# Performance work log

Measured on AMD Instinct MI355X. Metric: run time of the kernel, lower is better.

Reference implementation:

```python
import jax, jax.numpy as jnp
import numpy as np

N_NODES = 100000
N_EDGES = 3200000
NEG_SLOPE = 0.2  # PyG GATConv default


def setup_inputs() -> dict:
    key = jax.random.key(0)
    ks = jax.random.split(key, 10)
    g = 0.1
    return {
        "x": jax.random.normal(ks[0], (N_NODES, 3), jnp.float32),
        "edge_index": jax.random.randint(ks[1], (2, N_EDGES), 0, N_NODES),
        "w1": jax.random.normal(ks[2], (3, 32), jnp.float32) * g,
        "att_src1": jax.random.normal(ks[3], (2, 16), jnp.float32) * g,
        "att_dst1": jax.random.normal(ks[4], (2, 16), jnp.float32) * g,
        "b1": jnp.zeros((32,), jnp.float32),
        "w2": jax.random.normal(ks[5], (32, 14), jnp.float32) * g,
        "att_src2": jax.random.normal(ks[6], (2, 7), jnp.float32) * g,
        "att_dst2": jax.random.normal(ks[7], (2, 7), jnp.float32) * g,
        "b2": jnp.zeros((7,), jnp.float32),
    }


def _gat_conv(x, src, dst, W, att_src, att_dst, bias, heads, out_ch, concat, n):
    # x: [N, F_in]; src/dst: [E] (self-loops already appended)
    xl = (x @ W).reshape(n, heads, out_ch)          # [N, H, C]
    a_s = jnp.sum(xl * att_src[None], axis=-1)      # [N, H]
    a_d = jnp.sum(xl * att_dst[None], axis=-1)      # [N, H]
    alpha = jax.nn.leaky_relu(a_s[src] + a_d[dst], NEG_SLOPE)  # [E, H]
    # segment softmax over edges sharing a destination node
    mx = jax.ops.segment_max(alpha, dst, num_segments=n)        # [N, H]
    e = jnp.exp(alpha - mx[dst])
    denom = jax.ops.segment_sum(e, dst, num_segments=n)         # [N, H]
    alpha = e / (denom[dst] + 1e-16)
    msg = xl[src] * alpha[:, :, None]                            # [E, H, C]
    out = jax.ops.segment_sum(msg, dst, num_segments=n)         # [N, H, C]
    out = out.reshape(n, heads * out_ch) if concat else out.mean(axis=1)
    return out + bias


def reference(x, edge_index, w1, att_src1, att_dst1, b1, w2, att_src2, att_dst2, b2):
    n = x.shape[0]
    loop = jnp.arange(n)
    src = jnp.concatenate([edge_index[0], loop])  # add self-loops (PyG default)
    dst = jnp.concatenate([edge_index[1], loop])
    h = _gat_conv(x, src, dst, w1, att_src1, att_dst1, b1, 2, 16, True, n)
    h = jax.nn.relu(h)
    h = _gat_conv(h, src, dst, w2, att_src2, att_dst2, b2, 2, 7, False, n)
    return jax.nn.log_softmax(h, axis=1)
```

## Files before the change

kernel.cpp:

```cpp
#include <hip/hip_runtime.h>
#include <hip/hip_fp16.h>

static constexpr float NEG_SLOPE = 0.2f;
#define BUCKET_BITS 7
#define BNODES (1 << BUCKET_BITS)
#define MAXNB 1024
#define MAXSUP 32
#define SUPER_SHIFT 12
#define CHUNK1 2048
#define CHUNK 4096
#define PTHREADS 256
#define SORT_CAP 6144

__device__ __forceinline__ float2 h2f(float r) {
  return __half22float2(__builtin_bit_cast(__half2, r));
}

__global__ void k_node1(const float* __restrict__ x,
                        const float* __restrict__ w1,
                        const float* __restrict__ atts,
                        const float* __restrict__ attd,
                        float4* __restrict__ xp,
                        float* __restrict__ ad_,
                        unsigned* __restrict__ scur,
                        unsigned* __restrict__ bcur,
                        int n) {
  int i = blockIdx.x * blockDim.x + threadIdx.x;
  if (i < MAXSUP) scur[i] = 0u;
  if (i < MAXNB) bcur[i] = 0u;
  if (i >= n) return;
  float x0 = x[3*i], x1 = x[3*i+1], x2 = x[3*i+2];
  float v[32];
#pragma unroll
  for (int j = 0; j < 32; ++j)
    v[j] = fmaf(x0, w1[j], fmaf(x1, w1[32+j], x2 * w1[64+j]));
  float s0=0.f, s1=0.f, d0=0.f, d1=0.f;
#pragma unroll
  for (int k = 0; k < 16; ++k) {
    s0 = fmaf(v[k],    atts[k],    s0);
    d0 = fmaf(v[k],    attd[k],    d0);
    s1 = fmaf(v[16+k], atts[16+k], s1);
    d1 = fmaf(v[16+k], attd[16+k], d1);
  }
  float4 r;
  r.x = __builtin_bit_cast(float, __floats2half2_rn(x0, x1));
  r.y = __builtin_bit_cast(float, __floats2half2_rn(x2, s0));
  r.z = __builtin_bit_cast(float, __floats2half2_rn(s1, 0.f));
  r.w = 0.f;
  xp[i] = r;
  ad_[2*i] = d0; ad_[2*i+1] = d1;
}

__global__ void k_part1(const int* __restrict__ esrc, const int* __restrict__ edst,
                        unsigned* __restrict__ scur, unsigned* __restrict__ tmp1,
                        unsigned caps, int E) {
  __shared__ unsigned whist[4 * MAXSUP], wsub[4 * MAXSUP], woffs[4 * MAXSUP];
  int t = threadIdx.x;
  int w = t >> 6;
  for (int i = t; i < 4 * MAXSUP; i += PTHREADS) { whist[i] = 0u; woffs[i] = 0u; }
  __syncthreads();
  int e0 = blockIdx.x * CHUNK1;
  int e1 = min(E, e0 + CHUNK1);
  unsigned pkr[8], hir[8];
  int eb = e0 + t;
#pragma unroll
  for (int k = 0; k < 8; ++k) {
    int e = eb + k * PTHREADS;
    if (e < e1) {
      unsigned d = (unsigned)edst[e];
      unsigned s = (unsigned)esrc[e];
      unsigned hi = d >> SUPER_SHIFT;
      pkr[k] = (((d >> BUCKET_BITS) & 31u) << 24)
             | ((d & (BNODES - 1u)) << 17) | s;
      hir[k] = hi;
      atomicAdd(&whist[w * MAXSUP + hi], 1u);
    } else {
      hir[k] = 0xFFFFFFFFu;
    }
  }
  __syncthreads();
  if (t < MAXSUP) {
    unsigned h0 = whist[t],             h1 = whist[MAXSUP + t];
    unsigned h2 = whist[2*MAXSUP + t],  h3 = whist[3*MAXSUP + t];
    unsigned tot = h0 + h1 + h2 + h3;
    unsigned base = tot ? atomicAdd(&scur[t], tot) : 0u;
    wsub[t]            = base;
    wsub[MAXSUP + t]   = base + h0;
    wsub[2*MAXSUP + t] = base + h0 + h1;
    wsub[3*MAXSUP + t] = base + h0 + h1 + h2;
  }
  __syncthreads();
#pragma unroll
  for (int k = 0; k < 8; ++k) {
    unsigned hi = hir[k];
    if (hi != 0xFFFFFFFFu) {
      unsigned r = atomicAdd(&woffs[w * MAXSUP + hi], 1u);
      tmp1[(size_t)hi * caps + wsub[w * MAXSUP + hi] + r] = pkr[k];
    }
  }
}

__global__ void k_part2(const unsigned* __restrict__ tmp1,
                        const unsigned* __restrict__ scnt,
                        unsigned* __restrict__ bcur,
                        unsigned* __restrict__ packed2,
                        unsigned caps, unsigned capb, int maxch, int nb) {
  __shared__ unsigned stage[CHUNK];
  __shared__ unsigned hist[32], base[32], offs[32];
  int s = blockIdx.x / maxch;
  int c = blockIdx.x % maxch;
  unsigned count = scnt[s];
  int e0 = c * CHUNK;
  if ((unsigned)e0 >= count) return;
  int e1 = min((int)count, e0 + CHUNK);
  int t = threadIdx.x;
  if (t < 32) { hist[t] = 0u; offs[t] = 0u; }
  __syncthreads();
  const unsigned* src = tmp1 + (size_t)s * caps;
  for (int i = e0 + t; i < e1; i += PTHREADS) {
    unsigned pk = src[i];
    atomicAdd(&hist[pk >> 24], 1u);
    stage[i - e0] = pk;
  }
  __syncthreads();
  if (t < 32) {
    unsigned b = ((unsigned)s << 5) | (unsigned)t;
    if (hist[t] && b < (unsigned)nb) base[t] = atomicAdd(&bcur[b], hist[t]);
  }
  __syncthreads();
  for (int i = e0 + t; i < e1; i += PTHREADS) {
    unsigned pk = stage[i - e0];
    unsigned idx = pk >> 24;
    unsigned r = atomicAdd(&offs[idx], 1u);
    unsigned pos = base[idx] + r;
    unsigned b = ((unsigned)s << 5) | idx;
    if (pos < capb)
      packed2[(size_t)b * capb + pos] = pk & 0x00FFFFFFu;
  }
}

__global__ void k_sortb_g1(const unsigned* __restrict__ bcnt,
                           const unsigned* __restrict__ packed2,
                           const float4* __restrict__ xp,
                           const float* __restrict__ ad_,
                           int* __restrict__ col,
                           unsigned* __restrict__ rp,
                           unsigned* __restrict__ rend,
                           float4* __restrict__ numx,
                           unsigned capb, int n) {
  __shared__ unsigned stage_out[SORT_CAP];
  __shared__ unsigned cnt[BNODES], smi[BNODES], excl[BNODES], off[BNODES];
  int b = blockIdx.x;
  int size = (int)min(bcnt[b], capb);
  size_t bin = (size_t)b * capb;
  const unsigned* src = packed2 + bin;
  int base = b << BUCKET_BITS;
  int nNodes = min(BNODES, n - base);
  int t = threadIdx.x;
  if (t < BNODES) cnt[t] = 0u;
  __syncthreads();
  for (int i = t; i < size; i += 256)
    atomicAdd(&cnt[(src[i] >> 17) & 127u], 1u);
  __syncthreads();
  if (t < BNODES) smi[t] = cnt[t];
  __syncthreads();
#pragma unroll
  for (int offi = 1; offi < BNODES; offi <<= 1) {
    unsigned u = (t < BNODES && t >= offi) ? smi[t - offi] : 0u;
    __syncthreads();
    if (t < BNODES) smi[t] += u;
    __syncthreads();
  }
  if (t < BNODES) { unsigned e = smi[t] - cnt[t]; excl[t] = e; off[t] = e; }
  __syncthreads();
  for (int i = t; i < size; i += 256) {
    unsigned pk = src[i];
    unsigned slot = atomicAdd(&off[(pk >> 17) & 127u], 1u);
    stage_out[slot] = pk & 0x1FFFFu;
  }
  __syncthreads();
  for (int i = t; i < size; i += 256) col[bin + i] = (int)stage_out[i];
  if (t < nNodes) {
    unsigned r0 = (unsigned)bin + excl[t];
    rp[base + t] = r0;
    rend[base + t] = r0 + cnt[t];
  }
  int node = t >> 1, h = t & 1;
  if (node >= nNodes) return;
  float adh = ad_[(size_t)(base + node) * 2 + h];
  unsigned kb = excl[node], ke = kb + cnt[node];
  float4 acc = make_float4(0.f, 0.f, 0.f, 0.f);
  auto procr = [&](float4 r) {
    float2 fx01 = h2f(r.x);
    float2 fx2s = h2f(r.y);
    float2 fs1  = h2f(r.z);
    float as = h ? fs1.x : fx2s.y;
    float a = as + adh; a = (a >= 0.f) ? a : NEG_SLOPE * a;
    float e = __expf(a);
    acc.x = fmaf(fx01.x, e, acc.x);
    acc.y = fmaf(fx01.y, e, acc.y);
    acc.z = fmaf(fx2s.x, e, acc.z);
    acc.w += e;
  };
  unsigned k = kb;
  for (; k + 8 <= ke; k += 8) {
    unsigned i0 = stage_out[k],   i1 = stage_out[k+1];
    unsigned i2 = stage_out[k+2], i3 = stage_out[k+3];
    unsigned i4 = stage_out[k+4], i5 = stage_out[k+5];
    unsigned i6 = stage_out[k+6], i7 = stage_out[k+7];
    float4 r0 = xp[i0], r1 = xp[i1], r2 = xp[i2], r3 = xp[i3];
    float4 r4 = xp[i4], r5 = xp[i5], r6 = xp[i6], r7 = xp[i7];
    procr(r0); procr(r1); procr(r2); procr(r3);
    procr(r4); procr(r5); procr(r6); procr(r7);
  }
  for (; k < ke; ++k) procr(xp[stage_out[k]]);
  numx[(size_t)(base + node) * 2 + h] = acc;
}

__global__ void k_node2(const float* __restrict__ x,
                        const float4* __restrict__ numx,
                        const float* __restrict__ ad1,
                        const float* __restrict__ w1,
                        const float* __restrict__ atts1,
                        const float* __restrict__ b1,
                        const float* __restrict__ w2,
                        const float* __restrict__ atts2,
                        const float* __restrict__ attd2,
                        float4* __restrict__ xl2p,
                        float* __restrict__ ad2,
                        int n) {
  int i = blockIdx.x * blockDim.x + threadIdx.x;
  if (i >= n) return;
  float x0 = x[3*i], x1 = x[3*i+1], x2 = x[3*i+2];
  float v[32];
#pragma unroll
  for (int j = 0; j < 32; ++j)
    v[j] = fmaf(x0, w1[j], fmaf(x1, w1[32+j], x2 * w1[64+j]));
  float s0 = 0.f, s1 = 0.f;
#pragma unroll
  for (int k = 0; k < 16; ++k) {
    s0 = fmaf(v[k],    atts1[k],    s0);
    s1 = fmaf(v[16+k], atts1[16+k], s1);
  }
  float a0 = s0 + ad1[2*i];
  float a1 = s1 + ad1[2*i+1];
  a0 = (a0 >= 0.f) ? a0 : NEG_SLOPE * a0;
  a1 = (a1 >= 0.f) ? a1 : NEG_SLOPE * a1;
  float e0 = __expf(a0), e1 = __expf(a1);
  float4 nx0 = numx[2*i], nx1 = numx[2*i+1];
  float dh0 = nx0.w + e0 + 1e-16f;
  float dh1 = nx1.w + e1 + 1e-16f;
  float inv0 = 1.f / dh0, inv1 = 1.f / dh1;
  float hbuf[32];
#pragma unroll
  for (int j = 0; j < 16; ++j) {
    float nm = fmaf(nx0.x, w1[j], fmaf(nx0.y, w1[32+j], fmaf(nx0.z, w1[64+j], e0 * v[j])));
    float t = nm * inv0 + b1[j];
    hbuf[j] = t > 0.f ? t : 0.f;
  }
#pragma unroll
  for (int j = 0; j < 16; ++j) {
    int jj = 16 + j;
    float nm = fmaf(nx1.x, w1[jj], fmaf(nx1.y, w1[32+jj], fmaf(nx1.z, w1[64+jj], e1 * v[jj])));
    float t = nm * inv1 + b1[jj];
    hbuf[jj] = t > 0.f ? t : 0.f;
  }
  float o[14];
#pragma unroll
  for (int j = 0; j < 14; ++j) o[j] = 0.f;
#pragma unroll
  for (int ch = 0; ch < 32; ++ch) {
#pragma unroll
    for (int j = 0; j < 14; ++j)
      o[j] = fmaf(hbuf[ch], w2[14*ch + j], o[j]);
  }
  float t0=0.f, t1=0.f, d0=0.f, d1=0.f;
#pragma unroll
  for (int k = 0; k < 7; ++k) {
    t0 = fmaf(o[k],   atts2[k],   t0);
    d0 = fmaf(o[k],   attd2[k],   d0);
    t1 = fmaf(o[7+k], atts2[7+k], t1);
    d1 = fmaf(o[7+k], attd2[7+k], d1);
  }
  float4 rA, rB;
  rA.x = __builtin_bit_cast(float, __floats2half2_rn(o[0], o[1]));
  rA.y = __builtin_bit_cast(float, __floats2half2_rn(o[2], o[3]));
  rA.z = __builtin_bit_cast(float, __floats2half2_rn(o[4], o[5]));
  rA.w = __builtin_bit_cast(float, __floats2half2_rn(o[6], t0));
  rB.x = __builtin_bit_cast(float, __floats2half2_rn(o[7], o[8]));
  rB.y = __builtin_bit_cast(float, __floats2half2_rn(o[9], o[10]));
  rB.z = __builtin_bit_cast(float, __floats2half2_rn(o[11], o[12]));
  rB.w = __builtin_bit_cast(float, __floats2half2_rn(o[13], t1));
  xl2p[2*i]   = rA;
  xl2p[2*i+1] = rB;
  ad2[2*i] = d0; ad2[2*i+1] = d1;
}

__global__ void k_gather_final(const unsigned* __restrict__ rp,
                               const unsigned* __restrict__ rend,
                               const int* __restrict__ col,
                               const float4* __restrict__ xl2p,
                               const float* __restrict__ ad2,
                               const float* __restrict__ b2,
                               float* __restrict__ out,
                               int n) {
  int idx = blockIdx.x * blockDim.x + threadIdx.x;
  int d = idx >> 1;
  int h = idx & 1;
  if (d >= n) return;
  float adh = ad2[2*d + h];
  float acc[7] = {0.f,0.f,0.f,0.f,0.f,0.f,0.f};
  float den = 0.f;

  auto proc = [&](float4 r) {
    float2 c01 = h2f(r.x), c23 = h2f(r.y), c45 = h2f(r.z), c6a = h2f(r.w);
    float a = c6a.y + adh; a = (a >= 0.f) ? a : NEG_SLOPE*a;
    float e = __expf(a);
    acc[0] = fmaf(c01.x, e, acc[0]); acc[1] = fmaf(c01.y, e, acc[1]);
    acc[2] = fmaf(c23.x, e, acc[2]); acc[3] = fmaf(c23.y, e, acc[3]);
    acc[4] = fmaf(c45.x, e, acc[4]); acc[5] = fmaf(c45.y, e, acc[5]);
    acc[6] = fmaf(c6a.x, e, acc[6]); den += e;
  };

  unsigned jb = rp[d];
  unsigned je = rend[d];
  unsigned j = jb;
  for (; j + 8 <= je; j += 8) {
    int s0 = col[j],   s1 = col[j+1], s2 = col[j+2], s3 = col[j+3];
    int s4 = col[j+4], s5 = col[j+5], s6 = col[j+6], s7 = col[j+7];
    float4 r0 = xl2p[2*(size_t)s0 + h];
    float4 r1 = xl2p[2*(size_t)s1 + h];
    float4 r2 = xl2p[2*(size_t)s2 + h];
    float4 r3 = xl2p[2*(size_t)s3 + h];
    float4 r4 = xl2p[2*(size_t)s4 + h];
    float4 r5 = xl2p[2*(size_t)s5 + h];
    float4 r6 = xl2p[2*(size_t)s6 + h];
    float4 r7 = xl2p[2*(size_t)s7 + h];
    proc(r0); proc(r1); proc(r2); proc(r3);
    proc(r4); proc(r5); proc(r6); proc(r7);
  }
  for (; j < je; ++j) proc(xl2p[2*(size_t)col[j] + h]);
  proc(xl2p[2*(size_t)d + h]);

  float inv = 1.f / (den + 1e-16f);
  float v[7];
#pragma unroll
  for (int c = 0; c < 7; ++c) {
    float mine = acc[c] * inv;
    float other = __shfl_xor(mine, 1, 2);
    v[c] = 0.5f * (mine + other) + b2[c];
  }
  float m = v[0];
#pragma unroll
  for (int c = 1; c < 7; ++c) m = fmaxf(m, v[c]);
  float s = 0.f;
#pragma unroll
  for (int c = 0; c < 7; ++c) s += __expf(v[c] - m);
  float ls = __logf(s);
  float* o = out + (size_t)d * 7;
  if (h == 0) {
    o[0] = v[0]-m-ls; o[1] = v[1]-m-ls; o[2] = v[2]-m-ls; o[3] = v[3]-m-ls;
  } else {
    o[4] = v[4]-m-ls; o[5] = v[5]-m-ls; o[6] = v[6]-m-ls;
  }
}

extern "C" void kernel_launch(void* const* d_in, const int* in_sizes, int n_in,
                              void* d_out, int out_size, void* d_ws, size_t ws_size,
                              hipStream_t stream) {
  const float* x    = (const float*)d_in[0];
  const int*   ei   = (const int*)  d_in[1];
  const float* w1   = (const float*)d_in[2];
  const float* as1w = (const float*)d_in[3];
  const float* ad1w = (const float*)d_in[4];
  const float* b1   = (const float*)d_in[5];
  const float* w2   = (const float*)d_in[6];
  const float* as2w = (const float*)d_in[7];
  const float* ad2w = (const float*)d_in[8];
  const float* b2   = (const float*)d_in[9];
  float* out = (float*)d_out;

  const int n = in_sizes[0] / 3;
  const int E = in_sizes[1] / 2;
  const int* esrc = ei;
  const int* edst = ei + E;
  const int nb   = (n + BNODES - 1) >> BUCKET_BITS;
  const int nsup = (n + (1 << SUPER_SHIFT) - 1) >> SUPER_SHIFT;

  const unsigned avgb = (unsigned)(E / nb);
  const unsigned capb = (avgb + avgb / 16 + 384 + 7u) & ~7u;
  const unsigned avgs = (unsigned)(E / nsup);
  const unsigned caps = avgs + avgs / 16 + 4096;
  const int maxch = (int)((caps + CHUNK - 1) / CHUNK);

  const size_t Na = ((size_t)n + 3) & ~(size_t)3;
  float* ws = (float*)d_ws;
  float4* xp    = (float4*)ws;
  float*  ad1   = ws + 4*Na;
  float4* numx  = (float4*)(ws + 6*Na);
  float4* xl2p  = (float4*)(ws + 14*Na);
  float*  ad2   = ws + 22*Na;
  unsigned* ctrl   = (unsigned*)(ws + 24*Na);
  unsigned* scur   = ctrl;
  unsigned* bcur   = ctrl + MAXSUP;
  unsigned* rp     = bcur + MAXNB;
  unsigned* rend   = rp + Na;
  unsigned* packed2= rend + Na;
  int*      col    = (int*)(packed2 + (size_t)nb * capb);
  unsigned* tmp1   = (unsigned*)(col + (size_t)nb * capb);

  const int nbN = (n + 255) / 256;
  const int nbC1 = (E + CHUNK1 - 1) / CHUNK1;

  k_node1<<<nbN, 256, 0, stream>>>(x, w1, as1w, ad1w, xp, ad1, scur, bcur, n);

  k_part1<<<nbC1, PTHREADS, 0, stream>>>(esrc, edst, scur, tmp1, caps, E);
  k_part2<<<nsup * maxch, PTHREADS, 0, stream>>>(tmp1, scur, bcur, packed2,
                                                 caps, capb, maxch, nb);

  k_sortb_g1<<<nb, 256, 0, stream>>>(bcur, packed2, xp, ad1, col, rp, rend,
                                     numx, capb, n);

  k_node2<<<nbN, 256, 0, stream>>>(x, numx, ad1, w1, as1w, b1, w2,
                                   as2w, ad2w, xl2p, ad2, n);

  k_gather_final<<<(2*n + 255)/256, 256, 0, stream>>>(
      rp, rend, col, xl2p, ad2, b2, out, n);
}
```

Measured before the change: 132.3 us.

## Fuse layer-1 finalize and layer-2 projection into bucket sort/gather kernel

Removes the separate k_node2 launch and the numx intermediate buffer by running the layer-1 normalization, ReLU, W2 projection and attention dot products at the end of k_sortb_g1. Each thread of a (node, head) pair computes half of the 32-channel hidden vector and its partial 14-wide projection, and the two halves are combined with a lane shuffle. This saves one kernel launch and the numx write/read round trip. In exchange the sort kernel carries more register pressure and compute in its tail, which may lower its occupancy.

```diff
diff --git a/kernel.cpp b/kernel.cpp
--- a/kernel.cpp
+++ b/kernel.cpp
@@ -142,11 +142,19 @@
 __global__ void k_sortb_g1(const unsigned* __restrict__ bcnt,
                            const unsigned* __restrict__ packed2,
                            const float4* __restrict__ xp,
+                           const float* __restrict__ x,
                            const float* __restrict__ ad_,
+                           const float* __restrict__ w1,
+                           const float* __restrict__ atts1,
+                           const float* __restrict__ b1,
+                           const float* __restrict__ w2,
+                           const float* __restrict__ atts2,
+                           const float* __restrict__ attd2,
                            int* __restrict__ col,
                            unsigned* __restrict__ rp,
                            unsigned* __restrict__ rend,
-                           float4* __restrict__ numx,
+                           float4* __restrict__ xl2p,
+                           float* __restrict__ ad2,
                            unsigned capb, int n) {
   __shared__ unsigned stage_out[SORT_CAP];
   __shared__ unsigned cnt[BNODES], smi[BNODES], excl[BNODES], off[BNODES];
@@ -187,7 +195,8 @@
   }
   int node = t >> 1, h = t & 1;
   if (node >= nNodes) return;
-  float adh = ad_[(size_t)(base + node) * 2 + h];
+  int gnode = base + node;
+  float adh = ad_[(size_t)gnode * 2 + h];
   unsigned kb = excl[node], ke = kb + cnt[node];
   float4 acc = make_float4(0.f, 0.f, 0.f, 0.f);
   auto procr = [&](float4 r) {
@@ -214,86 +223,54 @@
     procr(r4); procr(r5); procr(r6); procr(r7);
   }
   for (; k < ke; ++k) procr(xp[stage_out[k]]);
-  numx[(size_t)(base + node) * 2 + h] = acc;
-}
-
-__global__ void k_node2(const float* __restrict__ x,
-                        const float4* __restrict__ numx,
-                        const float* __restrict__ ad1,
-                        const float* __restrict__ w1,
-                        const float* __restrict__ atts1,
-                        const float* __restrict__ b1,
-                        const float* __restrict__ w2,
-                        const float* __restrict__ atts2,
-                        const float* __restrict__ attd2,
-                        float4* __restrict__ xl2p,
-                        float* __restrict__ ad2,
-                        int n) {
-  int i = blockIdx.x * blockDim.x + threadIdx.x;
-  if (i >= n) return;
-  float x0 = x[3*i], x1 = x[3*i+1], x2 = x[3*i+2];
-  float v[32];
-#pragma unroll
-  for (int j = 0; j < 32; ++j)
-    v[j] = fmaf(x0, w1[j], fmaf(x1, w1[32+j], x2 * w1[64+j]));
-  float s0 = 0.f, s1 = 0.f;
-#pragma unroll
-  for (int k = 0; k < 16; ++k) {
-    s0 = fmaf(v[k],    atts1[k],    s0);
-    s1 = fmaf(v[16+k], atts1[16+k], s1);
-  }
-  float a0 = s0 + ad1[2*i];
-  float a1 = s1 + ad1[2*i+1];
-  a0 = (a0 >= 0.f) ? a0 : NEG_SLOPE * a0;
-  a1 = (a1 >= 0.f) ? a1 : NEG_SLOPE * a1;
-  float e0 = __expf(a0), e1 = __expf(a1);
-  float4 nx0 = numx[2*i], nx1 = numx[2*i+1];
-  float dh0 = nx0.w + e0 + 1e-16f;
-  float dh1 = nx1.w + e1 + 1e-16f;
-  float inv0 = 1.f / dh0, inv1 = 1.f / dh1;
-  float hbuf[32];
+  float x0 = x[3*gnode], x1 = x[3*gnode+1], x2 = x[3*gnode+2];
+  int cb = h << 4;
+  float v[16];
+#pragma unroll
+  for (int j = 0; j < 16; ++j)
+    v[j] = fmaf(x0, w1[cb+j], fmaf(x1, w1[32+cb+j], x2 * w1[64+cb+j]));
+  float sh = 0.f;
+#pragma unroll
+  for (int kk = 0; kk < 16; ++kk) sh = fmaf(v[kk], atts1[cb+kk], sh);
+  float ah = sh + adh;
+  ah = (ah >= 0.f) ? ah : NEG_SLOPE * ah;
+  float eh = __expf(ah);
+  float inv = 1.f / (acc.w + eh + 1e-16f);
+  float hbuf[16];
 #pragma unroll
   for (int j = 0; j < 16; ++j) {
-    float nm = fmaf(nx0.x, w1[j], fmaf(nx0.y, w1[32+j], fmaf(nx0.z, w1[64+j], e0 * v[j])));
-    float t = nm * inv0 + b1[j];
-    hbuf[j] = t > 0.f ? t : 0.f;
-  }
-#pragma unroll
-  for (int j = 0; j < 16; ++j) {
-    int jj = 16 + j;
-    float nm = fmaf(nx1.x, w1[jj], fmaf(nx1.y, w1[32+jj], fmaf(nx1.z, w1[64+jj], e1 * v[jj])));
-    float t = nm * inv1 + b1[jj];
-    hbuf[jj] = t > 0.f ? t : 0.f;
+    float nm = fmaf(acc.x, w1[cb+j],
+               fmaf(acc.y, w1[32+cb+j],
+               fmaf(acc.z, w1[64+cb+j], eh * v[j])));
+    float tv = nm * inv + b1[cb+j];
+    hbuf[j] = tv > 0.f ? tv : 0.f;
   }
   float o[14];
 #pragma unroll
   for (int j = 0; j < 14; ++j) o[j] = 0.f;
 #pragma unroll
-  for (int ch = 0; ch < 32; ++ch) {
+  for (int ch = 0; ch < 16; ++ch) {
 #pragma unroll
     for (int j = 0; j < 14; ++j)
-      o[j] = fmaf(hbuf[ch], w2[14*ch + j], o[j]);
-  }
-  float t0=0.f, t1=0.f, d0=0.f, d1=0.f;
-#pragma unroll
-  for (int k = 0; k < 7; ++k) {
-    t0 = fmaf(o[k],   atts2[k],   t0);
-    d0 = fmaf(o[k],   attd2[k],   d0);
-    t1 = fmaf(o[7+k], atts2[7+k], t1);
-    d1 = fmaf(o[7+k], attd2[7+k], d1);
-  }
-  float4 rA, rB;
-  rA.x = __builtin_bit_cast(float, __floats2half2_rn(o[0], o[1]));
-  rA.y = __builtin_bit_cast(float, __floats2half2_rn(o[2], o[3]));
-  rA.z = __builtin_bit_cast(float, __floats2half2_rn(o[4], o[5]));
-  rA.w = __builtin_bit_cast(float, __floats2half2_rn(o[6], t0));
-  rB.x = __builtin_bit_cast(float, __floats2half2_rn(o[7], o[8]));
-  rB.y = __builtin_bit_cast(float, __floats2half2_rn(o[9], o[10]));
-  rB.z = __builtin_bit_cast(float, __floats2half2_rn(o[11], o[12]));
-  rB.w = __builtin_bit_cast(float, __floats2half2_rn(o[13], t1));
-  xl2p[2*i]   = rA;
-  xl2p[2*i+1] = rB;
-  ad2[2*i] = d0; ad2[2*i+1] = d1;
+      o[j] = fmaf(hbuf[ch], w2[14*(cb+ch) + j], o[j]);
+  }
+#pragma unroll
+  for (int j = 0; j < 14; ++j)
+    o[j] += __shfl_xor(o[j], 1, 2);
+  int ob = 7 * h;
+  float th = 0.f, dh2 = 0.f;
+#pragma unroll
+  for (int kk = 0; kk < 7; ++kk) {
+    th  = fmaf(o[ob+kk], atts2[ob+kk], th);
+    dh2 = fmaf(o[ob+kk], attd2[ob+kk], dh2);
+  }
+  float4 rr;
+  rr.x = __builtin_bit_cast(float, __floats2half2_rn(o[ob+0], o[ob+1]));
+  rr.y = __builtin_bit_cast(float, __floats2half2_rn(o[ob+2], o[ob+3]));
+  rr.z = __builtin_bit_cast(float, __floats2half2_rn(o[ob+4], o[ob+5]));
+  rr.w = __builtin_bit_cast(float, __floats2half2_rn(o[ob+6], th));
+  xl2p[(size_t)gnode * 2 + h] = rr;
+  ad2[(size_t)gnode * 2 + h] = dh2;
 }
 
 __global__ void k_gather_final(const unsigned* __restrict__ rp,
@@ -397,10 +374,9 @@
   float* ws = (float*)d_ws;
   float4* xp    = (float4*)ws;
   float*  ad1   = ws + 4*Na;
-  float4* numx  = (float4*)(ws + 6*Na);
-  float4* xl2p  = (float4*)(ws + 14*Na);
-  float*  ad2   = ws + 22*Na;
-  unsigned* ctrl   = (unsigned*)(ws + 24*Na);
+  float4* xl2p  = (float4*)(ws + 6*Na);
+  float*  ad2   = ws + 14*Na;
+  unsigned* ctrl   = (unsigned*)(ws + 16*Na);
   unsigned* scur   = ctrl;
   unsigned* bcur   = ctrl + MAXSUP;
   unsigned* rp     = bcur + MAXNB;
@@ -418,11 +394,9 @@
   k_part2<<<nsup * maxch, PTHREADS, 0, stream>>>(tmp1, scur, bcur, packed2,
                                                  caps, capb, maxch, nb);
 
-  k_sortb_g1<<<nb, 256, 0, stream>>>(bcur, packed2, xp, ad1, col, rp, rend,
-                                     numx, capb, n);
-
-  k_node2<<<nbN, 256, 0, stream>>>(x, numx, ad1, w1, as1w, b1, w2,
-                                   as2w, ad2w, xl2p, ad2, n);
+  k_sortb_g1<<<nb, 256, 0, stream>>>(bcur, packed2, xp, x, ad1, w1, as1w, b1,
+                                     w2, as2w, ad2w, col, rp, rend,
+                                     xl2p, ad2, capb, n);
 
   k_gather_final<<<(2*n + 255)/256, 256, 0, stream>>>(
       rp, rend, col, xl2p, ad2, b2, out, n);
```

Measured after the change: 132.8 us. No clear change (+0.4%).
